# Kernel optimization log

Hardware: AMD Instinct MI355X
Metric: run time of the kernel (lower is better)

Reference implementation:

```python
import jax, jax.numpy as jnp
import numpy as np

_BN = 1.0 / np.sqrt(1.0 + 1e-5)  # eval-mode BatchNorm1d with default (fresh-init) stats/affine

def bn(z):
    return z * _BN

def lrelu(z, a):
    return jnp.where(z >= 0, z, a * z)

NEG = -9e15

def setup_inputs() -> dict:
    key = jax.random.key(0)
    ks = jax.random.split(key, 20)
    H = Wd = 256; B = 200; N = 2048; NHID = 128; OUT = 64; HEADS = 4
    x = jax.random.normal(ks[0], (H, Wd, B), dtype=jnp.float32)
    Q = jax.random.uniform(ks[1], (H * Wd, N), dtype=jnp.float32)
    adj = (jax.random.uniform(ks[2], (N, N)) < 0.02).astype(jnp.float32)
    adj = jnp.maximum(adj, jnp.eye(N, dtype=jnp.float32))  # self loops so no empty rows
    def u(k, shape, fan):
        s = 1.0 / np.sqrt(fan)
        return jax.random.uniform(k, shape, jnp.float32, -s, s)
    inp = dict(x=x, adj=adj, Q=Q)
    inp['g1a_W'] = u(ks[3], (B, NHID), NHID);  inp['g1a_b'] = u(ks[4], (NHID,), NHID)
    inp['g1b_W'] = u(ks[5], (NHID, B), B);     inp['g1b_b'] = u(ks[6], (B,), B)
    inp['g2a_W'] = u(ks[7], (B, NHID), NHID);  inp['g2a_b'] = u(ks[8], (NHID,), NHID)
    inp['g2b_W'] = u(ks[9], (NHID, OUT), OUT); inp['g2b_b'] = u(ks[10], (OUT,), OUT)
    inp['gat_W'] = jax.random.normal(ks[11], (HEADS, B, NHID)) * 0.1
    inp['gat_a'] = jax.random.normal(ks[12], (HEADS, 2 * NHID)) * 0.1
    inp['out_W'] = jax.random.normal(ks[13], (HEADS * NHID, OUT)) * 0.1
    inp['out_a'] = jax.random.normal(ks[14], (2 * OUT,)) * 0.1
    inp['Wf'] = u(ks[15], (2, OUT), OUT)
    inp['bf'] = u(ks[16], (2, OUT), OUT)
    inp['conv_w'] = jax.random.normal(ks[17], (3,)) * 0.5
    inp['conv_b'] = jax.random.normal(ks[18], (1,)) * 0.1
    return inp

def reference(x, adj, Q, g1a_W, g1a_b, g1b_W, g1b_b, g2a_W, g2a_b, g2b_W, g2b_b,
              gat_W, gat_a, out_W, out_a, Wf, bf, conv_w, conv_b):
    HW = x.shape[0] * x.shape[1]
    xf = x.reshape(HW, -1)                                   # [HW, C]
    normQ = Q / jnp.sum(Q, axis=0, keepdims=True)            # column-normalized assignment
    sp = normQ.T @ xf                                        # [N, C] superpixel features
    xn = bn(sp)

    # ---- Res_GCN branch ----
    def gcn_block(z, Wa, ba, Wb, bb):
        z = bn(z)
        z = lrelu(adj @ (z @ Wa) + ba, 0.01)
        z = bn(z)
        return adj @ (z @ Wb) + bb

    xg = bn(xn)
    y = lrelu(bn(gcn_block(xg, g1a_W, g1a_b, g1b_W, g1b_b)), 0.01)
    xg = xg + y
    GCN_x = lrelu(bn(gcn_block(xg, g2a_W, g2a_b, g2b_W, g2b_b)), 0.01)  # [N, OUT]

    # ---- GAT branch (fused pairwise scores: e_ij = lrelu(a1.Wh_i + a2.Wh_j)) ----
    mask = adj > 0
    nhid = gat_W.shape[2]

    def gat_head(Wk, ak):
        Wh = xn @ Wk                                         # [N, nhid]
        f1 = Wh @ ak[:nhid]                                  # [N]
        f2 = Wh @ ak[nhid:]                                  # [N]
        e = lrelu(f1[:, None] + f2[None, :], 0.2)            # [N, N]
        att = jax.nn.softmax(jnp.where(mask, e, NEG), axis=1)
        return jax.nn.elu(att @ Wh)                          # concat=True -> ELU

    heads = jax.vmap(gat_head)(gat_W, gat_a)                 # [H, N, nhid]
    hcat = jnp.moveaxis(heads, 0, 1).reshape(heads.shape[1], -1)  # [N, H*nhid]

    fo = out_W.shape[1]
    Wh = hcat @ out_W                                        # [N, OUT]
    e = lrelu((Wh @ out_a[:fo])[:, None] + (Wh @ out_a[fo:])[None, :], 0.2)
    att = jax.nn.softmax(jnp.where(mask, e, NEG), axis=1)
    GAT_x = lrelu(bn(jax.nn.elu(att @ Wh)), 0.01)            # [N, OUT]

    # ---- adaptive fusion ----
    mn = jnp.minimum(GCN_x, GAT_x)
    mx = jnp.maximum(GCN_x, GAT_x)
    avg = (GCN_x * Wf[0] + bf[0]) + (GAT_x * Wf[1] + bf[1])
    stk = jnp.stack([mn, mx, avg], axis=0)                   # [3, N, OUT]
    inp3 = stk + GAT_x + GCN_x                               # broadcast add
    y = jnp.einsum('c,cnf->nf', conv_w, inp3) + conv_b       # 1x1 conv 3->1 channels
    y = lrelu(bn(y), 0.2)                                    # AF2GNN1 leakyrelu(alpha)
    return Q @ y                                             # [HW, OUT]
```

## Files before the change

kernel.cpp:

```cpp
#include <hip/hip_runtime.h>
#include <math.h>

#define BNF 0.9999950000374997f

constexpr int N    = 2048;
constexpr int C    = 200;
constexpr int HW   = 65536;
constexpr int MAXDEG = 96;

typedef unsigned short u16;
typedef __attribute__((ext_vector_type(8))) short short8;
typedef __attribute__((ext_vector_type(4))) float f32x4;

union Frag  { short8 v; ushort4 h[2]; };
union FragA { short8 v; uint2 u2[2]; };

__device__ inline u16 f2bf(float x) {
    unsigned int u = __float_as_uint(x);
    unsigned int r = (u + 0x7fffu + ((u >> 16) & 1u)) >> 16;
    return (u16)r;
}

__device__ __forceinline__ void gload16(const void* g, void* l) {
    __builtin_amdgcn_global_load_lds(
        (const __attribute__((address_space(1))) unsigned int*)g,
        (__attribute__((address_space(3))) unsigned int*)l, 16, 0, 0);
}

__global__ __launch_bounds__(256) void k_convX(const float* __restrict__ xf,
                                               u16* __restrict__ xfT) {
    __shared__ __align__(16) u16 T2[200][140];
    const int i0 = blockIdx.x * 128;
    const int t = threadIdx.x;
    for (int p = 0; p < 25; ++p) {
        int idx = p * 256 + t;
        int il = idx / 50, cq = idx % 50;
        float4 v = *(const float4*)&xf[(size_t)(i0 + il) * 200 + cq * 4];
        T2[cq * 4 + 0][il] = f2bf(v.x);
        T2[cq * 4 + 1][il] = f2bf(v.y);
        T2[cq * 4 + 2][il] = f2bf(v.z);
        T2[cq * 4 + 3][il] = f2bf(v.w);
    }
    __syncthreads();
    for (int p = 0; p < 13; ++p) {
        int c = p * 16 + (t >> 4);
        if (c < 200) {
            int io = (t & 15) * 8;
            u16* dst = &xfT[(size_t)c * 65536 + i0 + io];
            *(ushort4*)&dst[0] = *(const ushort4*)&T2[c][io];
            *(ushort4*)&dst[4] = *(const ushort4*)&T2[c][io + 4];
        }
    }
    ushort4 z4 = {0, 0, 0, 0};
    for (int idx = t; idx < 56 * 16; idx += 256) {
        int r = 200 + (idx >> 4), io = (idx & 15) * 8;
        u16* dst = &xfT[(size_t)r * 65536 + i0 + io];
        *(ushort4*)&dst[0] = z4;
        *(ushort4*)&dst[4] = z4;
    }
}

__global__ __launch_bounds__(256, 2) void k_bigS(const float* __restrict__ Q,
                                                 const u16* __restrict__ xfT,
                                                 u16* __restrict__ Qbf,
                                                 float* __restrict__ S_part,
                                                 float* __restrict__ csPart) {
    __shared__ __align__(16) u16 Bt[2][256 * 32];
    __shared__ __align__(16) u16 At[128 * 34];
    const int bid = blockIdx.x;
    const int xcd = bid & 7, jj = bid >> 3;
    const int nt_b = jj & 15;
    const int ks_b = ((jj >> 4) << 3) + xcd;
    const int n0 = nt_b * 128;
    const size_t i0 = (size_t)ks_b * 2048;
    const int t = threadIdx.x, w = t >> 6, l = t & 63;
    const int ct0 = (w == 0) ? 0 : (4 + (w - 1) * 3);
    const int nct = (w == 0) ? 4 : 3;
    const int lrowB = l >> 2;
    const int scolB = (((l & 3) ^ ((l >> 3) & 3)) << 3);
    const int nq = t & 15;
    const int kp = t >> 4;

    f32x4 acc[8][4];
#pragma unroll
    for (int a = 0; a < 8; ++a)
#pragma unroll
        for (int b = 0; b < 4; ++b) acc[a][b] = (f32x4){0.f, 0.f, 0.f, 0.f};
    float csum[8] = {0.f, 0.f, 0.f, 0.f, 0.f, 0.f, 0.f, 0.f};

    float4 a0q[2], a0r[2], a1q[2], a1r[2];

#define ISSUE_B(PAR, STEP)                                                      \
    {                                                                           \
        const size_t kc = i0 + (size_t)(STEP) * 32 + scolB;                     \
        _Pragma("unroll")                                                       \
        for (int s = 0; s < 4; ++s) {                                           \
            const int seg = w + s * 4;                                          \
            gload16(&xfT[(size_t)(seg * 16 + lrowB) * 65536 + kc],              \
                    &Bt[PAR][seg * 512]);                                       \
        }                                                                       \
    }

#define LOAD_A(AQ, AR, STEP)                                                    \
    {                                                                           \
        const size_t r0 = (i0 + (size_t)(STEP) * 32 + kp * 2) * 2048;           \
        _Pragma("unroll")                                                       \
        for (int h = 0; h < 2; ++h) {                                           \
            const float* qp = &Q[r0 + n0 + h * 64 + nq * 4];                    \
            AQ[h] = *(const float4*)qp;                                         \
            AR[h] = *(const float4*)(qp + 2048);                                \
        }                                                                       \
    }

#define WRITE_A(AQ, AR, STEP)                                                   \
    {                                                                           \
        const size_t r0 = i0 + (size_t)(STEP) * 32 + kp * 2;                    \
        _Pragma("unroll")                                                       \
        for (int h = 0; h < 2; ++h) {                                           \
            const float* ca = (const float*)&AQ[h];                             \
            const float* cb = (const float*)&AR[h];                             \
            ushort4 s0, s1;                                                     \
            u16* q0 = (u16*)&s0; u16* q1 = (u16*)&s1;                           \
            _Pragma("unroll")                                                   \
            for (int j = 0; j < 4; ++j) {                                       \
                const int n_ = nq * 4 + h * 64 + j;                             \
                ushort2 p2;                                                     \
                p2.x = f2bf(ca[j]); p2.y = f2bf(cb[j]);                         \
                *(ushort2*)&At[n_ * 34 + ((n_ & 1) << 1) + kp * 2] = p2;        \
                csum[h * 4 + j] += ca[j] + cb[j];                               \
                q0[j] = p2.x; q1[j] = p2.y;                                     \
            }                                                                   \
            *(ushort4*)&Qbf[(size_t)r0 * 2048 + n0 + h * 64 + nq * 4] = s0;     \
            *(ushort4*)&Qbf[(size_t)(r0 + 1) * 2048 + n0 + h * 64 + nq * 4] = s1; \
        }                                                                       \
    }

#define MFMA_PHASE(PAR)                                                         \
    {                                                                           \
        const u16* Bb = Bt[PAR];                                                \
        const int g = l >> 4;                                                   \
        FragA af[8];                                                            \
        _Pragma("unroll")                                                       \
        for (int nt = 0; nt < 8; ++nt) {                                        \
            const int r = nt * 16 + (l & 15);                                   \
            const int ab = r * 34 + ((r & 1) << 1) + g * 8;                     \
            af[nt].u2[0] = *(const uint2*)&At[ab];                              \
            af[nt].u2[1] = *(const uint2*)&At[ab + 4];                          \
        }                                                                       \
        _Pragma("unroll")                                                       \
        for (int c = 0; c < 4; ++c) {                                           \
            if (c < nct) {                                                      \
                const int rb = (ct0 + c) * 16 + (l & 15);                       \
                Frag bf;                                                        \
                bf.v = *(const short8*)&Bb[rb * 32 + ((g ^ ((rb >> 1) & 3)) << 3)]; \
                _Pragma("unroll")                                               \
                for (int nt = 0; nt < 8; ++nt)                                  \
                    acc[nt][c] = __builtin_amdgcn_mfma_f32_16x16x32_bf16(       \
                        af[nt].v, bf.v, acc[nt][c], 0, 0, 0);                   \
            }                                                                   \
        }                                                                       \
    }

#define STEPBODY(STEP, PAR, NPAR, CQ, CR, NQr, NRr, COND)                       \
    {                                                                           \
        if (COND) ISSUE_B(NPAR, (STEP) + 1);                                    \
        WRITE_A(CQ, CR, STEP);                                                  \
        if (COND) LOAD_A(NQr, NRr, (STEP) + 1);                                 \
        asm volatile("s_waitcnt lgkmcnt(0)" ::: "memory");                      \
        __builtin_amdgcn_s_barrier();                                           \
        if (COND) { asm volatile("s_waitcnt vmcnt(12)" ::: "memory"); }         \
        else      { asm volatile("s_waitcnt vmcnt(0)"  ::: "memory"); }         \
        MFMA_PHASE(PAR);                                                        \
        __builtin_amdgcn_s_barrier();                                           \
    }

    ISSUE_B(0, 0);
    LOAD_A(a0q, a0r, 0);

    for (int s2 = 0; s2 < 32; ++s2) {
        STEPBODY(s2 * 2,     0, 1, a0q, a0r, a1q, a1r, true);
        STEPBODY(s2 * 2 + 1, 1, 0, a1q, a1r, a0q, a0r, (s2 < 31));
    }
#undef STEPBODY
#undef MFMA_PHASE
#undef WRITE_A
#undef LOAD_A
#undef ISSUE_B

    __syncthreads();
    float* csF = (float*)At;
#pragma unroll
    for (int h = 0; h < 2; ++h)
#pragma unroll
        for (int j = 0; j < 4; ++j)
            csF[kp * 128 + nq * 4 + h * 64 + j] = csum[h * 4 + j];
    __syncthreads();
    if (t < 128) {
        float s = 0.f;
#pragma unroll
        for (int g2 = 0; g2 < 16; ++g2) s += csF[g2 * 128 + t];
        csPart[(size_t)ks_b * 2048 + n0 + t] = s;
    }
    float* Sp = S_part + (size_t)ks_b * 409600;
#pragma unroll
    for (int nt = 0; nt < 8; ++nt)
#pragma unroll
        for (int c = 0; c < 4; ++c) {
            if (c < nct) {
                const int cc = (ct0 + c) * 16 + (l & 15);
                if (cc < 200) {
                    const int nbase = n0 + nt * 16 + ((l >> 4) << 2);
#pragma unroll
                    for (int r = 0; r < 4; ++r)
                        Sp[(size_t)(nbase + r) * 200 + cc] = acc[nt][c][r];
                }
            }
        }
}

__global__ void k_csum(const float* __restrict__ csPart, float* __restrict__ cs) {
    int n = blockIdx.x * 256 + threadIdx.x;
    float s = 0.f;
#pragma unroll 8
    for (int p = 0; p < 32; ++p) s += csPart[(size_t)p * 2048 + n];
    cs[n] = s;
}

__global__ void k_redS(const float* __restrict__ S_part, const float* __restrict__ cs,
                       float* __restrict__ xn, float* __restrict__ xg) {
    int i = blockIdx.x * 256 + threadIdx.x;
    if (i >= N * C) return;
    float s = 0.f;
#pragma unroll 8
    for (int p = 0; p < 32; ++p) s += S_part[(size_t)p * 409600 + i];
    int n = i / C;
    float v = BNF * s / cs[n];
    xn[i] = v;
    xg[i] = BNF * v;
}

__global__ void k_csr(const float* __restrict__ adj, int* __restrict__ deg,
                      int* __restrict__ idxs) {
    int w = threadIdx.x >> 6, lane = threadIdx.x & 63;
    int n = blockIdx.x * 4 + w;
    const float* row = adj + (size_t)n * N;
    int base = 0;
    for (int c = 0; c < N; c += 64) {
        float v = row[c + lane];
        bool p = v > 0.f;
        unsigned long long m = __ballot(p);
        int pos = __popcll(m & ((1ull << lane) - 1ull));
        if (p && (base + pos) < MAXDEG) idxs[(size_t)n * MAXDEG + base + pos] = c + lane;
        base += __popcll(m);
    }
    if (lane == 0) deg[n] = base < MAXDEG ? base : MAXDEG;
}

__global__ __launch_bounds__(256) void k_mm(const float* __restrict__ A,
                                            const float* __restrict__ W,
                                            float* __restrict__ Cc,
                                            int K, int Wout, int ostride,
                                            int zc_off, int zw_str, float scale) {
    __shared__ float ldsA[32][33];
    __shared__ float ldsW[32][64];
    const int rt = blockIdx.x * 32;
    const int ct = blockIdx.y * 64;
    const int z  = blockIdx.z;
    const float* Wp = W + (size_t)z * zw_str;
    const int coff = z * zc_off;
    const int t = threadIdx.x;
    const int lane = t & 63, wg = t >> 6;
    float acc[8];
#pragma unroll
    for (int r = 0; r < 8; ++r) acc[r] = 0.f;

    for (int k0 = 0; k0 < K; k0 += 32) {
        for (int idx = t; idx < 32 * 32; idx += 256) {
            int r = idx >> 5, kk = idx & 31;
            int k = k0 + kk;
            ldsA[r][kk] = (k < K) ? A[(size_t)(rt + r) * K + k] : 0.f;
        }
        for (int idx = t; idx < 32 * 64; idx += 256) {
            int kk = idx >> 6, c = idx & 63;
            int k = k0 + kk, cg = ct + c;
            ldsW[kk][c] = (k < K && cg < Wout) ? Wp[(size_t)k * Wout + cg] : 0.f;
        }
        __syncthreads();
#pragma unroll 8
        for (int kk = 0; kk < 32; ++kk) {
            float wv = ldsW[kk][lane];
#pragma unroll
            for (int r = 0; r < 8; ++r) acc[r] += ldsA[wg * 8 + r][kk] * wv;
        }
        __syncthreads();
    }
    int cg = ct + lane;
    if (cg < Wout) {
#pragma unroll
        for (int r = 0; r < 8; ++r)
            Cc[(size_t)(rt + wg * 8 + r) * ostride + coff + cg] = scale * acc[r];
    }
}

__global__ void k_spmm(const float* __restrict__ h, const int* __restrict__ deg,
                       const int* __restrict__ idxs, const float* __restrict__ bias,
                       const float* __restrict__ res, float* __restrict__ out,
                       int W, float s, int act) {
    int n = blockIdx.x;
    int d = deg[n];
    const int* row = idxs + (size_t)n * MAXDEG;
    int k0 = threadIdx.x;
    int k1 = threadIdx.x + 128;
    float a0 = 0.f, a1 = 0.f;
    for (int j = 0; j < d; ++j) {
        const float* hr = h + (size_t)row[j] * W;
        a0 += hr[k0];
        if (k1 < W) a1 += hr[k1];
    }
    {
        float v = s * (a0 + bias[k0]);
        if (act) v = v >= 0.f ? v : 0.01f * v;
        if (res) v += res[(size_t)n * W + k0];
        out[(size_t)n * W + k0] = v;
    }
    if (k1 < W) {
        float v = s * (a1 + bias[k1]);
        if (act) v = v >= 0.f ? v : 0.01f * v;
        if (res) v += res[(size_t)n * W + k1];
        out[(size_t)n * W + k1] = v;
    }
}

__global__ __launch_bounds__(256) void k_gatWh(const float* __restrict__ xn,
                                               const float* __restrict__ gatW,
                                               const float* __restrict__ gata,
                                               float* __restrict__ WhB,
                                               float* __restrict__ f1,
                                               float* __restrict__ f2) {
    __shared__ float ldsA[32][33];
    __shared__ float ldsW[32][128];
    __shared__ float ldsWh[32][129];
    const int rt = blockIdx.x * 32;
    const int h  = blockIdx.y;
    const float* Wp = gatW + (size_t)h * 200 * 128;
    const int t = threadIdx.x;
    const int col = t & 127, rg = t >> 7;
    float acc[16];
#pragma unroll
    for (int r = 0; r < 16; ++r) acc[r] = 0.f;

    for (int k0 = 0; k0 < 200; k0 += 32) {
        for (int idx = t; idx < 32 * 32; idx += 256) {
            int r = idx >> 5, kk = idx & 31;
            int k = k0 + kk;
            ldsA[r][kk] = (k < 200) ? xn[(size_t)(rt + r) * 200 + k] : 0.f;
        }
        for (int idx = t; idx < 32 * 128; idx += 256) {
            int kk = idx >> 7, c = idx & 127;
            int k = k0 + kk;
            ldsW[kk][c] = (k < 200) ? Wp[(size_t)k * 128 + c] : 0.f;
        }
        __syncthreads();
#pragma unroll 8
        for (int kk = 0; kk < 32; ++kk) {
            float wv = ldsW[kk][col];
#pragma unroll
            for (int r = 0; r < 16; ++r) acc[r] += ldsA[rg * 16 + r][kk] * wv;
        }
        __syncthreads();
    }
#pragma unroll
    for (int r = 0; r < 16; ++r) {
        ldsWh[rg * 16 + r][col] = acc[r];
        WhB[(size_t)(rt + rg * 16 + r) * 512 + h * 128 + col] = acc[r];
    }
    __syncthreads();
    int row = t >> 3, p = t & 7;
    const float* a = gata + h * 256;
    float s1 = 0.f, s2 = 0.f;
#pragma unroll
    for (int j = 0; j < 16; ++j) {
        int c = p * 16 + j;
        float v = ldsWh[row][c];
        s1 += v * a[c]; s2 += v * a[128 + c];
    }
    s1 += __shfl_xor(s1, 1); s1 += __shfl_xor(s1, 2); s1 += __shfl_xor(s1, 4);
    s2 += __shfl_xor(s2, 1); s2 += __shfl_xor(s2, 2); s2 += __shfl_xor(s2, 4);
    if (p == 0) { f1[h * N + rt + row] = s1; f2[h * N + rt + row] = s2; }
}

__global__ void k_att_head(const float* __restrict__ WhB, const float* __restrict__ f1,
                           const float* __restrict__ f2, const int* __restrict__ deg,
                           const int* __restrict__ idxs, float* __restrict__ hcat) {
    int n = blockIdx.x, h = blockIdx.y;
    int k = threadIdx.x;
    int d = deg[n];
    const int* row = idxs + (size_t)n * MAXDEG;
    float f1v = f1[h * N + n];
    const float* f2h = f2 + h * N;
    float mx = -1e30f;
    for (int j = 0; j < d; ++j) {
        float e = f1v + f2h[row[j]];
        e = e >= 0.f ? e : 0.2f * e;
        mx = fmaxf(mx, e);
    }
    float ssum = 0.f, acc = 0.f;
    for (int j = 0; j < d; ++j) {
        int m = row[j];
        float e = f1v + f2h[m];
        e = e >= 0.f ? e : 0.2f * e;
        float w = __expf(e - mx);
        ssum += w;
        acc += w * WhB[(size_t)m * 512 + h * 128 + k];
    }
    float v = acc / ssum;
    v = v > 0.f ? v : __expf(v) - 1.f;
    hcat[(size_t)n * 512 + h * 128 + k] = v;
}

__global__ __launch_bounds__(256) void k_mmO(const float* __restrict__ hcat,
                                             const float* __restrict__ outW,
                                             const float* __restrict__ outa,
                                             float* __restrict__ WhO,
                                             float* __restrict__ f1o,
                                             float* __restrict__ f2o) {
    __shared__ float ldsA[32][33];
    __shared__ float ldsW[32][64];
    const int rt = blockIdx.x * 32;
    const int t = threadIdx.x;
    const int lane = t & 63, wg = t >> 6;
    float acc[8];
#pragma unroll
    for (int r = 0; r < 8; ++r) acc[r] = 0.f;

    for (int k0 = 0; k0 < 512; k0 += 32) {
        for (int idx = t; idx < 32 * 32; idx += 256) {
            int r = idx >> 5, kk = idx & 31;
            ldsA[r][kk] = hcat[(size_t)(rt + r) * 512 + k0 + kk];
        }
        for (int idx = t; idx < 32 * 64; idx += 256) {
            int kk = idx >> 6, c = idx & 63;
            ldsW[kk][c] = outW[(size_t)(k0 + kk) * 64 + c];
        }
        __syncthreads();
#pragma unroll 8
        for (int kk = 0; kk < 32; ++kk) {
            float wv = ldsW[kk][lane];
#pragma unroll
            for (int r = 0; r < 8; ++r) acc[r] += ldsA[wg * 8 + r][kk] * wv;
        }
        __syncthreads();
    }
#pragma unroll
    for (int r = 0; r < 8; ++r)
        WhO[(size_t)(rt + wg * 8 + r) * 64 + lane] = acc[r];
#pragma unroll
    for (int r = 0; r < 8; ++r) {
        float v1 = acc[r] * outa[lane];
        float v2 = acc[r] * outa[64 + lane];
#pragma unroll
        for (int off = 32; off; off >>= 1) {
            v1 += __shfl_down(v1, off);
            v2 += __shfl_down(v2, off);
        }
        if (lane == 0) { f1o[rt + wg * 8 + r] = v1; f2o[rt + wg * 8 + r] = v2; }
    }
}

__global__ void k_att_out(const float* __restrict__ WhO, const float* __restrict__ f1o,
                          const float* __restrict__ f2o, const int* __restrict__ deg,
                          const int* __restrict__ idxs, const float* __restrict__ GCNx,
                          const float* __restrict__ Wf, const float* __restrict__ bfp,
                          const float* __restrict__ cw, const float* __restrict__ cb,
                          u16* __restrict__ yT) {
    int n = blockIdx.x;
    int k = threadIdx.x;
    int d = deg[n];
    const int* row = idxs + (size_t)n * MAXDEG;
    float f1v = f1o[n];
    float mx = -1e30f;
    for (int j = 0; j < d; ++j) {
        float e = f1v + f2o[row[j]];
        e = e >= 0.f ? e : 0.2f * e;
        mx = fmaxf(mx, e);
    }
    float ssum = 0.f, acc = 0.f;
    for (int j = 0; j < d; ++j) {
        int m = row[j];
        float e = f1v + f2o[m];
        e = e >= 0.f ? e : 0.2f * e;
        float w = __expf(e - mx);
        ssum += w;
        acc += w * WhO[(size_t)m * 64 + k];
    }
    float v = acc / ssum;
    v = v > 0.f ? v : __expf(v) - 1.f;
    v *= BNF;
    float gat = v >= 0.f ? v : 0.01f * v;
    float g = GCNx[(size_t)n * 64 + k];
    float mn = fminf(g, gat), mxv = fmaxf(g, gat);
    float avg = g * Wf[k] + bfp[k] + gat * Wf[64 + k] + bfp[64 + k];
    float base = g + gat;
    float yv = cw[0] * (mn + base) + cw[1] * (mxv + base) + cw[2] * (avg + base) + cb[0];
    yv *= BNF;
    yv = yv >= 0.f ? yv : 0.2f * yv;
    yT[k * 2048 + n] = f2bf(yv);
}

__global__ __launch_bounds__(256, 2) void k_final(const u16* __restrict__ Qbf,
                                                  const u16* __restrict__ yT,
                                                  float* __restrict__ out) {
    __shared__ __align__(16) u16 Aq[2][128 * 64];
    __shared__ __align__(16) u16 By[2][64 * 64];
    const int i0 = blockIdx.x * 128;
    const int t = threadIdx.x, w = t >> 6, l = t & 63;
    const int lrow = l >> 3;
    const int scol = (((l & 7) ^ ((l >> 3) & 7)) << 3);
    f32x4 acc[2][4];
#pragma unroll
    for (int a = 0; a < 2; ++a)
#pragma unroll
        for (int b = 0; b < 4; ++b) acc[a][b] = (f32x4){0.f, 0.f, 0.f, 0.f};

#define STAGE_F(buf, step)                                                          \
    {                                                                               \
        const size_t kc = (size_t)(step) * 64 + scol;                               \
        for (int s = w; s < 16; s += 4)                                             \
            gload16(&Qbf[(size_t)(i0 + s * 8 + lrow) * 2048 + kc],                  \
                    &Aq[buf][s * 512]);                                             \
        for (int s = w; s < 8; s += 4)                                              \
            gload16(&yT[(size_t)(s * 8 + lrow) * 2048 + kc],                        \
                    &By[buf][s * 512]);                                             \
    }

    STAGE_F(0, 0);
    for (int step = 0; step < 32; ++step) {
        const int cur = step & 1;
        if (step + 1 < 32) {
            STAGE_F(cur ^ 1, step + 1);
            asm volatile("s_waitcnt vmcnt(6)" ::: "memory");
        } else {
            asm volatile("s_waitcnt vmcnt(0)" ::: "memory");
        }
        __builtin_amdgcn_s_barrier();

        const u16* Ab = Aq[cur];
        const u16* Bb = By[cur];
#pragma unroll
        for (int sub = 0; sub < 2; ++sub) {
            const int c8 = sub * 4 + (l >> 4);
            Frag a[2];
#pragma unroll
            for (int it = 0; it < 2; ++it) {
                const int r = w * 32 + it * 16 + (l & 15);
                a[it].v = *(const short8*)&Ab[r * 64 + ((c8 ^ (r & 7)) << 3)];
            }
#pragma unroll
            for (int ft = 0; ft < 4; ++ft) {
                const int rb = ft * 16 + (l & 15);
                Frag b;
                b.v = *(const short8*)&Bb[rb * 64 + ((c8 ^ (rb & 7)) << 3)];
#pragma unroll
                for (int it = 0; it < 2; ++it)
                    acc[it][ft] = __builtin_amdgcn_mfma_f32_16x16x32_bf16(
                        a[it].v, b.v, acc[it][ft], 0, 0, 0);
            }
        }
        asm volatile("s_waitcnt lgkmcnt(0)" ::: "memory");
        __builtin_amdgcn_s_barrier();
    }
#undef STAGE_F
#pragma unroll
    for (int it = 0; it < 2; ++it)
#pragma unroll
        for (int ft = 0; ft < 4; ++ft) {
            const int i = i0 + w * 32 + it * 16 + ((l >> 4) << 2);
            const int f = ft * 16 + (l & 15);
#pragma unroll
            for (int r = 0; r < 4; ++r)
                out[(size_t)(i + r) * 64 + f] = acc[it][ft][r];
        }
}

extern "C" void kernel_launch(void* const* d_in, const int* in_sizes, int n_in,
                              void* d_out, int out_size, void* d_ws, size_t ws_size,
                              hipStream_t stream) {
    const float* x     = (const float*)d_in[0];
    const float* adj   = (const float*)d_in[1];
    const float* Q     = (const float*)d_in[2];
    const float* g1aW  = (const float*)d_in[3];
    const float* g1ab  = (const float*)d_in[4];
    const float* g1bW  = (const float*)d_in[5];
    const float* g1bb  = (const float*)d_in[6];
    const float* g2aW  = (const float*)d_in[7];
    const float* g2ab  = (const float*)d_in[8];
    const float* g2bW  = (const float*)d_in[9];
    const float* g2bb  = (const float*)d_in[10];
    const float* gatW  = (const float*)d_in[11];
    const float* gata  = (const float*)d_in[12];
    const float* outW  = (const float*)d_in[13];
    const float* outa  = (const float*)d_in[14];
    const float* Wf    = (const float*)d_in[15];
    const float* bfp   = (const float*)d_in[16];
    const float* convw = (const float*)d_in[17];
    const float* convb = (const float*)d_in[18];

    float* ws   = (float*)d_ws;
    float* cs   = ws + 409600;
    float* xn   = ws + 411648;
    float* xg   = ws + 821248;
    float* xg2  = ws + 1230848;
    float* hbuf = ws + 1640448;
    float* zbuf = ws + 2050048;
    float* WhO  = ws + 2312192;
    float* GCNx = ws + 2443264;
    float* f1   = ws + 2836480;
    float* f2   = ws + 2844672;
    float* f1o  = ws + 2852864;
    float* f2o  = ws + 2854912;
    int*   deg  = (int*)(ws + 2856960);
    int*   idxs = (int*)(ws + 2859008);
    u16*   yT   = (u16*)(ws + 1640448);
    float* csPart = ws + 3000000;
    float* S_part = ws + 4200000;
    u16*   Qbf    = (u16*)(ws + 71308864);
    u16*   xfT    = (u16*)(ws + 138417728);

    float* out  = (float*)d_out;
    float* WhB  = out;
    float* hcat = out + 1048576;

    k_convX<<<512, 256, 0, stream>>>(x, xfT);
    k_bigS<<<512, 256, 0, stream>>>(Q, xfT, Qbf, S_part, csPart);
    k_csum<<<8, 256, 0, stream>>>(csPart, cs);
    k_redS<<<(N * C + 255) / 256, 256, 0, stream>>>(S_part, cs, xn, xg);
    k_csr<<<N / 4, 256, 0, stream>>>(adj, deg, idxs);

    k_mm<<<dim3(64, 2, 1), 256, 0, stream>>>(xg, g1aW, hbuf, 200, 128, 128, 0, 0, BNF);
    k_spmm<<<N, 128, 0, stream>>>(hbuf, deg, idxs, g1ab, nullptr, zbuf, 128, 1.f, 1);
    k_mm<<<dim3(64, 4, 1), 256, 0, stream>>>(zbuf, g1bW, hbuf, 128, 200, 200, 0, 0, BNF);
    k_spmm<<<N, 128, 0, stream>>>(hbuf, deg, idxs, g1bb, xg, xg2, 200, BNF, 1);
    k_mm<<<dim3(64, 2, 1), 256, 0, stream>>>(xg2, g2aW, hbuf, 200, 128, 128, 0, 0, BNF);
    k_spmm<<<N, 128, 0, stream>>>(hbuf, deg, idxs, g2ab, nullptr, zbuf, 128, 1.f, 1);
    k_mm<<<dim3(64, 1, 1), 256, 0, stream>>>(zbuf, g2bW, hbuf, 128, 64, 64, 0, 0, BNF);
    k_spmm<<<N, 64, 0, stream>>>(hbuf, deg, idxs, g2bb, nullptr, GCNx, 64, BNF, 1);

    k_gatWh<<<dim3(64, 4), 256, 0, stream>>>(xn, gatW, gata, WhB, f1, f2);
    k_att_head<<<dim3(N, 4), 128, 0, stream>>>(WhB, f1, f2, deg, idxs, hcat);
    k_mmO<<<64, 256, 0, stream>>>(hcat, outW, outa, WhO, f1o, f2o);

    k_att_out<<<N, 64, 0, stream>>>(WhO, f1o, f2o, deg, idxs, GCNx,
                                    Wf, bfp, convw, convb, yT);

    k_final<<<512, 256, 0, stream>>>(Qbf, yT, out);
}
```

Before: 726.4 us.

## Retile big S GEMM, fold column-sum into reduce, merge first GCN matmul into GAT Wh

The big Q^T·x GEMM now uses 64-column N tiles with 1024 blocks, 13 B segments (208 rows instead of 256) and 3 blocks per SM, so it loads less zero padding and keeps more blocks resident. The separate column-sum kernel is folded into the S reduction, and the first GCN matmul is computed alongside the four GAT head projections in one launch using xn scaled by BNF². Attention kernels stage the edge scores in shared memory instead of recomputing them, and launches are reordered to interleave the independent branches. The changes trade larger grids and extra shared-memory barriers for less redundant work, and the tighter vmcnt waits depend on the new per-wave load counts being right.

```diff
diff --git a/kernel.cpp b/kernel.cpp
--- a/kernel.cpp
+++ b/kernel.cpp
@@ -52,7 +52,7 @@
         }
     }
     ushort4 z4 = {0, 0, 0, 0};
-    for (int idx = t; idx < 56 * 16; idx += 256) {
+    for (int idx = t; idx < 8 * 16; idx += 256) {
         int r = 200 + (idx >> 4), io = (idx & 15) * 8;
         u16* dst = &xfT[(size_t)r * 65536 + i0 + io];
         *(ushort4*)&dst[0] = z4;
@@ -60,18 +60,18 @@
     }
 }
 
-__global__ __launch_bounds__(256, 2) void k_bigS(const float* __restrict__ Q,
+__global__ __launch_bounds__(256, 3) void k_bigS(const float* __restrict__ Q,
                                                  const u16* __restrict__ xfT,
                                                  u16* __restrict__ Qbf,
                                                  float* __restrict__ S_part,
                                                  float* __restrict__ csPart) {
-    __shared__ __align__(16) u16 Bt[2][256 * 32];
-    __shared__ __align__(16) u16 At[128 * 34];
+    __shared__ __align__(16) u16 Bt[2][208 * 32];
+    __shared__ __align__(16) u16 At[64 * 34];
     const int bid = blockIdx.x;
-    const int xcd = bid & 7, jj = bid >> 3;
-    const int nt_b = jj & 15;
-    const int ks_b = ((jj >> 4) << 3) + xcd;
-    const int n0 = nt_b * 128;
+    const int xcd = bid & 7, jb = bid >> 3;
+    const int nt_b = jb & 31;
+    const int ks_b = ((jb >> 5) << 3) + xcd;
+    const int n0 = nt_b * 64;
     const size_t i0 = (size_t)ks_b * 2048;
     const int t = threadIdx.x, w = t >> 6, l = t & 63;
     const int ct0 = (w == 0) ? 0 : (4 + (w - 1) * 3);
@@ -81,67 +81,58 @@
     const int nq = t & 15;
     const int kp = t >> 4;
 
-    f32x4 acc[8][4];
-#pragma unroll
-    for (int a = 0; a < 8; ++a)
+    f32x4 acc[4][4];
+#pragma unroll
+    for (int a = 0; a < 4; ++a)
 #pragma unroll
         for (int b = 0; b < 4; ++b) acc[a][b] = (f32x4){0.f, 0.f, 0.f, 0.f};
-    float csum[8] = {0.f, 0.f, 0.f, 0.f, 0.f, 0.f, 0.f, 0.f};
-
-    float4 a0q[2], a0r[2], a1q[2], a1r[2];
+    float csum[4] = {0.f, 0.f, 0.f, 0.f};
+
+    float4 aq0, ar0, aq1, ar1;
 
 #define ISSUE_B(PAR, STEP)                                                      \
     {                                                                           \
         const size_t kc = i0 + (size_t)(STEP) * 32 + scolB;                     \
-        _Pragma("unroll")                                                       \
-        for (int s = 0; s < 4; ++s) {                                           \
-            const int seg = w + s * 4;                                          \
-            gload16(&xfT[(size_t)(seg * 16 + lrowB) * 65536 + kc],              \
-                    &Bt[PAR][seg * 512]);                                       \
-        }                                                                       \
+        for (int s = w; s < 13; s += 4)                                         \
+            gload16(&xfT[(size_t)(s * 16 + lrowB) * 65536 + kc],                \
+                    &Bt[PAR][s * 512]);                                         \
     }
 
 #define LOAD_A(AQ, AR, STEP)                                                    \
     {                                                                           \
-        const size_t r0 = (i0 + (size_t)(STEP) * 32 + kp * 2) * 2048;           \
-        _Pragma("unroll")                                                       \
-        for (int h = 0; h < 2; ++h) {                                           \
-            const float* qp = &Q[r0 + n0 + h * 64 + nq * 4];                    \
-            AQ[h] = *(const float4*)qp;                                         \
-            AR[h] = *(const float4*)(qp + 2048);                                \
-        }                                                                       \
+        const float* qp = &Q[(i0 + (size_t)(STEP) * 32 + kp * 2) * 2048         \
+                             + n0 + nq * 4];                                    \
+        AQ = *(const float4*)qp;                                                \
+        AR = *(const float4*)(qp + 2048);                                       \
     }
 
 #define WRITE_A(AQ, AR, STEP)                                                   \
     {                                                                           \
+        const float* ca = (const float*)&AQ;                                    \
+        const float* cb = (const float*)&AR;                                    \
+        ushort4 s0, s1;                                                         \
+        u16* q0 = (u16*)&s0; u16* q1 = (u16*)&s1;                               \
+        _Pragma("unroll")                                                       \
+        for (int jj = 0; jj < 4; ++jj) {                                        \
+            const int n_ = nq * 4 + jj;                                         \
+            ushort2 p2;                                                         \
+            p2.x = f2bf(ca[jj]); p2.y = f2bf(cb[jj]);                           \
+            *(ushort2*)&At[n_ * 34 + ((n_ & 1) << 1) + kp * 2] = p2;            \
+            csum[jj] += ca[jj] + cb[jj];                                        \
+            q0[jj] = p2.x; q1[jj] = p2.y;                                       \
+        }                                                                       \
         const size_t r0 = i0 + (size_t)(STEP) * 32 + kp * 2;                    \
-        _Pragma("unroll")                                                       \
-        for (int h = 0; h < 2; ++h) {                                           \
-            const float* ca = (const float*)&AQ[h];                             \
-            const float* cb = (const float*)&AR[h];                             \
-            ushort4 s0, s1;                                                     \
-            u16* q0 = (u16*)&s0; u16* q1 = (u16*)&s1;                           \
-            _Pragma("unroll")                                                   \
-            for (int j = 0; j < 4; ++j) {                                       \
-                const int n_ = nq * 4 + h * 64 + j;                             \
-                ushort2 p2;                                                     \
-                p2.x = f2bf(ca[j]); p2.y = f2bf(cb[j]);                         \
-                *(ushort2*)&At[n_ * 34 + ((n_ & 1) << 1) + kp * 2] = p2;        \
-                csum[h * 4 + j] += ca[j] + cb[j];                               \
-                q0[j] = p2.x; q1[j] = p2.y;                                     \
-            }                                                                   \
-            *(ushort4*)&Qbf[(size_t)r0 * 2048 + n0 + h * 64 + nq * 4] = s0;     \
-            *(ushort4*)&Qbf[(size_t)(r0 + 1) * 2048 + n0 + h * 64 + nq * 4] = s1; \
-        }                                                                       \
+        *(ushort4*)&Qbf[r0 * 2048 + n0 + nq * 4] = s0;                          \
+        *(ushort4*)&Qbf[(r0 + 1) * 2048 + n0 + nq * 4] = s1;                    \
     }
 
 #define MFMA_PHASE(PAR)                                                         \
     {                                                                           \
         const u16* Bb = Bt[PAR];                                                \
         const int g = l >> 4;                                                   \
-        FragA af[8];                                                            \
+        FragA af[4];                                                            \
         _Pragma("unroll")                                                       \
-        for (int nt = 0; nt < 8; ++nt) {                                        \
+        for (int nt = 0; nt < 4; ++nt) {                                        \
             const int r = nt * 16 + (l & 15);                                   \
             const int ab = r * 34 + ((r & 1) << 1) + g * 8;                     \
             af[nt].u2[0] = *(const uint2*)&At[ab];                              \
@@ -154,7 +145,7 @@
                 Frag bf;                                                        \
                 bf.v = *(const short8*)&Bb[rb * 32 + ((g ^ ((rb >> 1) & 3)) << 3)]; \
                 _Pragma("unroll")                                               \
-                for (int nt = 0; nt < 8; ++nt)                                  \
+                for (int nt = 0; nt < 4; ++nt)                                  \
                     acc[nt][c] = __builtin_amdgcn_mfma_f32_16x16x32_bf16(       \
                         af[nt].v, bf.v, acc[nt][c], 0, 0, 0);                   \
             }                                                                   \
@@ -168,18 +159,22 @@
         if (COND) LOAD_A(NQr, NRr, (STEP) + 1);                                 \
         asm volatile("s_waitcnt lgkmcnt(0)" ::: "memory");                      \
         __builtin_amdgcn_s_barrier();                                           \
-        if (COND) { asm volatile("s_waitcnt vmcnt(12)" ::: "memory"); }         \
-        else      { asm volatile("s_waitcnt vmcnt(0)"  ::: "memory"); }         \
+        if (COND) {                                                             \
+            if (w == 0) asm volatile("s_waitcnt vmcnt(8)" ::: "memory");        \
+            else        asm volatile("s_waitcnt vmcnt(7)" ::: "memory");        \
+        } else {                                                                \
+            asm volatile("s_waitcnt vmcnt(0)" ::: "memory");                    \
+        }                                                                       \
         MFMA_PHASE(PAR);                                                        \
         __builtin_amdgcn_s_barrier();                                           \
     }
 
     ISSUE_B(0, 0);
-    LOAD_A(a0q, a0r, 0);
+    LOAD_A(aq0, ar0, 0);
 
     for (int s2 = 0; s2 < 32; ++s2) {
-        STEPBODY(s2 * 2,     0, 1, a0q, a0r, a1q, a1r, true);
-        STEPBODY(s2 * 2 + 1, 1, 0, a1q, a1r, a0q, a0r, (s2 < 31));
+        STEPBODY(s2 * 2,     0, 1, aq0, ar0, aq1, ar1, true);
+        STEPBODY(s2 * 2 + 1, 1, 0, aq1, ar1, aq0, ar0, (s2 < 31));
     }
 #undef STEPBODY
 #undef MFMA_PHASE
@@ -190,20 +185,18 @@
     __syncthreads();
     float* csF = (float*)At;
 #pragma unroll
-    for (int h = 0; h < 2; ++h)
-#pragma unroll
-        for (int j = 0; j < 4; ++j)
-            csF[kp * 128 + nq * 4 + h * 64 + j] = csum[h * 4 + j];
-    __syncthreads();
-    if (t < 128) {
+    for (int jj = 0; jj < 4; ++jj)
+        csF[kp * 64 + nq * 4 + jj] = csum[jj];
+    __syncthreads();
+    if (t < 64) {
         float s = 0.f;
 #pragma unroll
-        for (int g2 = 0; g2 < 16; ++g2) s += csF[g2 * 128 + t];
+        for (int g2 = 0; g2 < 16; ++g2) s += csF[g2 * 64 + t];
         csPart[(size_t)ks_b * 2048 + n0 + t] = s;
     }
     float* Sp = S_part + (size_t)ks_b * 409600;
 #pragma unroll
-    for (int nt = 0; nt < 8; ++nt)
+    for (int nt = 0; nt < 4; ++nt)
 #pragma unroll
         for (int c = 0; c < 4; ++c) {
             if (c < nct) {
@@ -218,23 +211,17 @@
         }
 }
 
-__global__ void k_csum(const float* __restrict__ csPart, float* __restrict__ cs) {
-    int n = blockIdx.x * 256 + threadIdx.x;
-    float s = 0.f;
-#pragma unroll 8
-    for (int p = 0; p < 32; ++p) s += csPart[(size_t)p * 2048 + n];
-    cs[n] = s;
-}
-
-__global__ void k_redS(const float* __restrict__ S_part, const float* __restrict__ cs,
+__global__ void k_redS(const float* __restrict__ S_part, const float* __restrict__ csPart,
                        float* __restrict__ xn, float* __restrict__ xg) {
     int i = blockIdx.x * 256 + threadIdx.x;
     if (i >= N * C) return;
-    float s = 0.f;
+    int n = i / C;
+    float s = 0.f, csn = 0.f;
 #pragma unroll 8
     for (int p = 0; p < 32; ++p) s += S_part[(size_t)p * 409600 + i];
-    int n = i / C;
-    float v = BNF * s / cs[n];
+#pragma unroll 8
+    for (int p = 0; p < 32; ++p) csn += csPart[(size_t)p * 2048 + n];
+    float v = BNF * s / csn;
     xn[i] = v;
     xg[i] = BNF * v;
 }
@@ -331,18 +318,21 @@
     }
 }
 
-__global__ __launch_bounds__(256) void k_gatWh(const float* __restrict__ xn,
-                                               const float* __restrict__ gatW,
-                                               const float* __restrict__ gata,
-                                               float* __restrict__ WhB,
-                                               float* __restrict__ f1,
-                                               float* __restrict__ f2) {
+__global__ __launch_bounds__(256) void k_wh5(const float* __restrict__ xn,
+                                             const float* __restrict__ gatW,
+                                             const float* __restrict__ gata,
+                                             const float* __restrict__ g1aW,
+                                             float* __restrict__ WhB,
+                                             float* __restrict__ f1,
+                                             float* __restrict__ f2,
+                                             float* __restrict__ hbuf) {
     __shared__ float ldsA[32][33];
     __shared__ float ldsW[32][128];
     __shared__ float ldsWh[32][129];
     const int rt = blockIdx.x * 32;
-    const int h  = blockIdx.y;
-    const float* Wp = gatW + (size_t)h * 200 * 128;
+    const int z  = blockIdx.y;
+    const bool gat = z < 4;
+    const float* Wp = gat ? gatW + (size_t)z * 25600 : g1aW;
     const int t = threadIdx.x;
     const int col = t & 127, rg = t >> 7;
     float acc[16];
@@ -369,50 +359,57 @@
         }
         __syncthreads();
     }
-#pragma unroll
-    for (int r = 0; r < 16; ++r) {
-        ldsWh[rg * 16 + r][col] = acc[r];
-        WhB[(size_t)(rt + rg * 16 + r) * 512 + h * 128 + col] = acc[r];
-    }
-    __syncthreads();
-    int row = t >> 3, p = t & 7;
-    const float* a = gata + h * 256;
-    float s1 = 0.f, s2 = 0.f;
-#pragma unroll
-    for (int j = 0; j < 16; ++j) {
-        int c = p * 16 + j;
-        float v = ldsWh[row][c];
-        s1 += v * a[c]; s2 += v * a[128 + c];
-    }
-    s1 += __shfl_xor(s1, 1); s1 += __shfl_xor(s1, 2); s1 += __shfl_xor(s1, 4);
-    s2 += __shfl_xor(s2, 1); s2 += __shfl_xor(s2, 2); s2 += __shfl_xor(s2, 4);
-    if (p == 0) { f1[h * N + rt + row] = s1; f2[h * N + rt + row] = s2; }
+    if (gat) {
+#pragma unroll
+        for (int r = 0; r < 16; ++r) {
+            ldsWh[rg * 16 + r][col] = acc[r];
+            WhB[(size_t)(rt + rg * 16 + r) * 512 + z * 128 + col] = acc[r];
+        }
+        __syncthreads();
+        int row = t >> 3, p = t & 7;
+        const float* a = gata + z * 256;
+        float s1 = 0.f, s2 = 0.f;
+#pragma unroll
+        for (int j = 0; j < 16; ++j) {
+            int c = p * 16 + j;
+            float v = ldsWh[row][c];
+            s1 += v * a[c]; s2 += v * a[128 + c];
+        }
+        s1 += __shfl_xor(s1, 1); s1 += __shfl_xor(s1, 2); s1 += __shfl_xor(s1, 4);
+        s2 += __shfl_xor(s2, 1); s2 += __shfl_xor(s2, 2); s2 += __shfl_xor(s2, 4);
+        if (p == 0) { f1[z * N + rt + row] = s1; f2[z * N + rt + row] = s2; }
+    } else {
+        const float sc = BNF * BNF;
+#pragma unroll
+        for (int r = 0; r < 16; ++r)
+            hbuf[(size_t)(rt + rg * 16 + r) * 128 + col] = sc * acc[r];
+    }
 }
 
 __global__ void k_att_head(const float* __restrict__ WhB, const float* __restrict__ f1,
                            const float* __restrict__ f2, const int* __restrict__ deg,
                            const int* __restrict__ idxs, float* __restrict__ hcat) {
+    __shared__ float eW[MAXDEG];
     int n = blockIdx.x, h = blockIdx.y;
     int k = threadIdx.x;
     int d = deg[n];
     const int* row = idxs + (size_t)n * MAXDEG;
     float f1v = f1[h * N + n];
     const float* f2h = f2 + h * N;
+    if (k < d) {
+        float e = f1v + f2h[row[k]];
+        eW[k] = e >= 0.f ? e : 0.2f * e;
+    }
+    __syncthreads();
     float mx = -1e30f;
-    for (int j = 0; j < d; ++j) {
-        float e = f1v + f2h[row[j]];
-        e = e >= 0.f ? e : 0.2f * e;
-        mx = fmaxf(mx, e);
-    }
+    for (int j = 0; j < d; ++j) mx = fmaxf(mx, eW[j]);
+    __syncthreads();
+    if (k < d) eW[k] = __expf(eW[k] - mx);
+    __syncthreads();
     float ssum = 0.f, acc = 0.f;
-    for (int j = 0; j < d; ++j) {
-        int m = row[j];
-        float e = f1v + f2h[m];
-        e = e >= 0.f ? e : 0.2f * e;
-        float w = __expf(e - mx);
-        ssum += w;
-        acc += w * WhB[(size_t)m * 512 + h * 128 + k];
-    }
+    for (int j = 0; j < d; ++j) ssum += eW[j];
+    for (int j = 0; j < d; ++j)
+        acc += eW[j] * WhB[(size_t)row[j] * 512 + h * 128 + k];
     float v = acc / ssum;
     v = v > 0.f ? v : __expf(v) - 1.f;
     hcat[(size_t)n * 512 + h * 128 + k] = v;
@@ -473,26 +470,26 @@
                           const float* __restrict__ Wf, const float* __restrict__ bfp,
                           const float* __restrict__ cw, const float* __restrict__ cb,
                           u16* __restrict__ yT) {
+    __shared__ float eW[MAXDEG];
     int n = blockIdx.x;
     int k = threadIdx.x;
     int d = deg[n];
     const int* row = idxs + (size_t)n * MAXDEG;
     float f1v = f1o[n];
+    for (int j = k; j < d; j += 64) {
+        float e = f1v + f2o[row[j]];
+        eW[j] = e >= 0.f ? e : 0.2f * e;
+    }
+    __syncthreads();
     float mx = -1e30f;
-    for (int j = 0; j < d; ++j) {
-        float e = f1v + f2o[row[j]];
-        e = e >= 0.f ? e : 0.2f * e;
-        mx = fmaxf(mx, e);
-    }
+    for (int j = 0; j < d; ++j) mx = fmaxf(mx, eW[j]);
+    __syncthreads();
+    for (int j = k; j < d; j += 64) eW[j] = __expf(eW[j] - mx);
+    __syncthreads();
     float ssum = 0.f, acc = 0.f;
-    for (int j = 0; j < d; ++j) {
-        int m = row[j];
-        float e = f1v + f2o[m];
-        e = e >= 0.f ? e : 0.2f * e;
-        float w = __expf(e - mx);
-        ssum += w;
-        acc += w * WhO[(size_t)m * 64 + k];
-    }
+    for (int j = 0; j < d; ++j) ssum += eW[j];
+    for (int j = 0; j < d; ++j)
+        acc += eW[j] * WhO[(size_t)row[j] * 64 + k];
     float v = acc / ssum;
     v = v > 0.f ? v : __expf(v) - 1.f;
     v *= BNF;
@@ -507,7 +504,7 @@
     yT[k * 2048 + n] = f2bf(yv);
 }
 
-__global__ __launch_bounds__(256, 2) void k_final(const u16* __restrict__ Qbf,
+__global__ __launch_bounds__(256, 3) void k_final(const u16* __restrict__ Qbf,
                                                   const u16* __restrict__ yT,
                                                   float* __restrict__ out) {
     __shared__ __align__(16) u16 Aq[2][128 * 64];
@@ -606,7 +603,6 @@
     const float* convb = (const float*)d_in[18];
 
     float* ws   = (float*)d_ws;
-    float* cs   = ws + 409600;
     float* xn   = ws + 411648;
     float* xg   = ws + 821248;
     float* xg2  = ws + 1230848;
@@ -631,24 +627,22 @@
     float* hcat = out + 1048576;
 
     k_convX<<<512, 256, 0, stream>>>(x, xfT);
-    k_bigS<<<512, 256, 0, stream>>>(Q, xfT, Qbf, S_part, csPart);
-    k_csum<<<8, 256, 0, stream>>>(csPart, cs);
-    k_redS<<<(N * C + 255) / 256, 256, 0, stream>>>(S_part, cs, xn, xg);
+    k_bigS<<<1024, 256, 0, stream>>>(Q, xfT, Qbf, S_part, csPart);
+    k_redS<<<(N * C + 255) / 256, 256, 0, stream>>>(S_part, csPart, xn, xg);
     k_csr<<<N / 4, 256, 0, stream>>>(adj, deg, idxs);
 
-    k_mm<<<dim3(64, 2, 1), 256, 0, stream>>>(xg, g1aW, hbuf, 200, 128, 128, 0, 0, BNF);
+    k_wh5<<<dim3(64, 5), 256, 0, stream>>>(xn, gatW, gata, g1aW, WhB, f1, f2, hbuf);
+
     k_spmm<<<N, 128, 0, stream>>>(hbuf, deg, idxs, g1ab, nullptr, zbuf, 128, 1.f, 1);
+    k_att_head<<<dim3(N, 4), 128, 0, stream>>>(WhB, f1, f2, deg, idxs, hcat);
     k_mm<<<dim3(64, 4, 1), 256, 0, stream>>>(zbuf, g1bW, hbuf, 128, 200, 200, 0, 0, BNF);
+    k_mmO<<<64, 256, 0, stream>>>(hcat, outW, outa, WhO, f1o, f2o);
     k_spmm<<<N, 128, 0, stream>>>(hbuf, deg, idxs, g1bb, xg, xg2, 200, BNF, 1);
     k_mm<<<dim3(64, 2, 1), 256, 0, stream>>>(xg2, g2aW, hbuf, 200, 128, 128, 0, 0, BNF);
     k_spmm<<<N, 128, 0, stream>>>(hbuf, deg, idxs, g2ab, nullptr, zbuf, 128, 1.f, 1);
     k_mm<<<dim3(64, 1, 1), 256, 0, stream>>>(zbuf, g2bW, hbuf, 128, 64, 64, 0, 0, BNF);
     k_spmm<<<N, 64, 0, stream>>>(hbuf, deg, idxs, g2bb, nullptr, GCNx, 64, BNF, 1);
 
-    k_gatWh<<<dim3(64, 4), 256, 0, stream>>>(xn, gatW, gata, WhB, f1, f2);
-    k_att_head<<<dim3(N, 4), 128, 0, stream>>>(WhB, f1, f2, deg, idxs, hcat);
-    k_mmO<<<64, 256, 0, stream>>>(hcat, outW, outa, WhO, f1o, f2o);
-
     k_att_out<<<N, 64, 0, stream>>>(WhO, f1o, f2o, deg, idxs, GCNx,
                                     Wf, bfp, convw, convb, yT);
 
```

Result: no change. 724.6 us (-0.3%).
